# Kernel optimization log

Hardware: AMD Instinct MI355X
Metric: run time of the kernel (lower is better)

## Reference

```python
import jax, jax.numpy as jnp
import numpy as np

B = 8          # batch
S = 256        # nx+1 = ny+1 grid resolution
N = S * S      # number of DoFs per component
DIM = 2        # output vector dimension (= d_out)
W = 32         # FNO channel width
M1 = 12        # Fourier modes dim 1
M2 = 12        # Fourier modes dim 2
WF = 128       # final MLP hidden width
NL = 4         # number of Fourier layers
PADF = 8       # padding fraction denominator


def setup_inputs() -> dict:
    key = jax.random.key(0)
    ks = jax.random.split(key, 16)
    sc = 1.0 / (W * W)  # torch FNO spectral weight init scale
    return {
        "x": jax.random.normal(ks[0], (B, N), jnp.float32),
        "d2v_in": jax.random.permutation(ks[1], jnp.arange(N)),
        "v2d_out": jax.random.permutation(ks[2], jnp.arange(N)),
        "fc0_w": jax.random.normal(ks[3], (W, 3), jnp.float32) * 0.1,
        "fc0_b": jnp.zeros((W,), jnp.float32),
        "spec_w1r": jax.random.uniform(ks[4], (NL, W, W, M1, M2), jnp.float32) * sc,
        "spec_w1i": jax.random.uniform(ks[5], (NL, W, W, M1, M2), jnp.float32) * sc,
        "spec_w2r": jax.random.uniform(ks[6], (NL, W, W, M1, M2), jnp.float32) * sc,
        "spec_w2i": jax.random.uniform(ks[7], (NL, W, W, M1, M2), jnp.float32) * sc,
        "conv_w": jax.random.normal(ks[8], (NL, W, W), jnp.float32) * 0.05,
        "conv_b": jnp.zeros((NL, W), jnp.float32),
        "mlp_w1": jax.random.normal(ks[9], (WF, W), jnp.float32) * 0.05,
        "mlp_b1": jnp.zeros((WF,), jnp.float32),
        "mlp_w2": jax.random.normal(ks[10], (DIM, WF), jnp.float32) * 0.05,
        "mlp_b2": jnp.zeros((DIM,), jnp.float32),
    }


def _speconv(x, w1, w2):
    # x: (B, C, H, Wd) real; w1/w2: (C_in, C_out, M1, M2) complex64
    Bh, C, H, Wd = x.shape
    xft = jnp.fft.rfft2(x)  # (B, C, H, Wd//2+1)
    o1 = jnp.einsum('bixy,ioxy->boxy', xft[:, :, :M1, :M2], w1)
    o2 = jnp.einsum('bixy,ioxy->boxy', xft[:, :, -M1:, :M2], w2)
    out_ft = jnp.zeros((Bh, C, H, Wd // 2 + 1), jnp.complex64)
    out_ft = out_ft.at[:, :, :M1, :M2].set(o1).at[:, :, -M1:, :M2].set(o2)
    return jnp.fft.irfft2(out_ft, s=(H, Wd))


def reference(x, d2v_in, v2d_out, fc0_w, fc0_b,
              spec_w1r, spec_w1i, spec_w2r, spec_w2i,
              conv_w, conv_b, mlp_w1, mlp_b1, mlp_w2, mlp_b2):
    # DoF -> vertex gather and lift to image
    xg = x[:, d2v_in].reshape(B, 1, S, S)
    h = jnp.transpose(xg, (0, 2, 3, 1))  # (B, S, S, 1)
    # append normalized grid coordinates (get_grid2d)
    g = jnp.linspace(0.0, 1.0, S, dtype=jnp.float32)
    grid = jnp.stack(jnp.meshgrid(g, g, indexing='ij'), axis=-1)  # (S, S, 2)
    grid = jnp.broadcast_to(grid[None], (B, S, S, 2))
    h = jnp.concatenate([h, grid], axis=-1)
    # fc0 lifting
    h = h @ fc0_w.T + fc0_b              # (B, S, S, W)
    h = jnp.transpose(h, (0, 3, 1, 2))   # (B, W, S, S)
    # zero pad (non-periodic domain)
    p = S // PADF
    h = jnp.pad(h, ((0, 0), (0, 0), (0, p), (0, p)))  # (B, W, S+p, S+p)
    w1 = (spec_w1r + 1j * spec_w1i).astype(jnp.complex64)
    w2 = (spec_w2r + 1j * spec_w2i).astype(jnp.complex64)
    for l in range(NL):
        sp = _speconv(h, w1[l], w2[l])
        cv = jnp.einsum('bchw,oc->bohw', h, conv_w[l]) + conv_b[l][None, :, None, None]
        h = cv + sp
        if l != NL - 1:
            h = jax.nn.gelu(h, approximate=False)  # torch GELU default = exact erf
    # crop padding (s_outputspace=None path)
    h = h[..., :S, :S]
    # final two-layer MLP projection
    h = jnp.transpose(h, (0, 2, 3, 1))  # (B, S, S, W)
    h = jax.nn.gelu(h @ mlp_w1.T + mlp_b1, approximate=False) @ mlp_w2.T + mlp_b2
    h = jnp.transpose(h, (0, 3, 1, 2)).reshape(B, DIM, -1)  # (B, DIM, N)
    # vertex -> DoF scatter/gather and interleave components
    out = h[:, :, v2d_out]              # (B, DIM, N)
    out = jnp.transpose(out, (0, 2, 1)).reshape(B, -1)  # (B, N*DIM)
    return out
```

## Files before the change

### kernel.cpp

```cpp
#include <hip/hip_runtime.h>
#include <math.h>

#define S    256
#define Hp   288
#define C    32
#define KY   12
#define NK   24
#define Bn   8
#define PI_D 3.14159265358979323846264338327950288

#define SZ_TW (NK*Hp*2)
#define OFF_TW 0
#define OFF_H  (OFF_TW + SZ_TW)
#define SZ_H   (Bn*C*Hp*Hp)
#define OFF_Y  (OFF_H + SZ_H)
#define SZ_Y   (Bn*C*Hp*KY*2)
#define OFF_X  (OFF_Y + SZ_Y)
#define SZ_X   (Bn*C*NK*KY*2)
#define OFF_O  (OFF_X + SZ_X)
#define SZ_O   SZ_X
#define OFF_Z  (OFF_O + SZ_O)
#define SZ_Z   (Bn*Hp*C*KY*2)
#define OFF_T  (OFF_Z + SZ_Z)
#define SZ_T   (Bn*S*S*2)

#define GELU(v) (0.5f*(v)*(1.0f+erff((v)*0.70710678118654752f)))
#define SCHED_FENCE() __builtin_amdgcn_sched_barrier(0)

__global__ void k_tw(float* __restrict__ tw) {
    int i = blockIdx.x * 256 + threadIdx.x;
    if (i >= NK * Hp) return;
    int k = i / Hp, xx = i % Hp;
    int f = (k < KY) ? k : (k + 264);
    int m = (f * xx) % Hp;
    double th = (2.0 * PI_D * (double)m) / (double)Hp;
    tw[2 * i]     = (float)cos(th);
    tw[2 * i + 1] = (float)sin(th);
}

__global__ __launch_bounds__(256, 1) void k_embed(
        const float* __restrict__ xin, const int* __restrict__ d2v,
        const float* __restrict__ fw, const float* __restrict__ fb,
        const float* __restrict__ tw, float* __restrict__ h, float* __restrict__ Y) {
    __shared__ __align__(16) float xs[256];
    __shared__ __align__(16) float twy[288 * 24];
    int x = blockIdx.x, b = blockIdx.y, tid = threadIdx.x;
    size_t rowbase = (size_t)b * 2654208 + (size_t)x * 288;
    if (x >= S) {
        for (int i = tid; i < 32 * 72; i += 256) {
            int c = i / 72, q = i % 72;
            *(float4*)&h[rowbase + (size_t)c * 82944 + q * 4] = make_float4(0, 0, 0, 0);
        }
        for (int i = tid; i < 768; i += 256)
            Y[((size_t)(b * 32 + i / 24) * 288 + x) * 24 + (i % 24)] = 0.f;
        return;
    }
    for (int i = tid; i < 288 * 12; i += 256) {
        int y = i / 12, k = i % 12;
        float2 v = *(const float2*)&tw[(k * 288 + y) * 2];
        *(float2*)&twy[y * 24 + 2 * k] = v;
    }
    xs[tid & 255] = xin[b * 65536 + d2v[x * 256 + (tid & 255)]];
    int o = tid & 31, g = tid >> 5;
    float w0 = fw[o * 3], w1 = fw[o * 3 + 1], w2 = fw[o * 3 + 2], bb = fb[o];
    float gx = x * (1.0f / 255.0f);
    __syncthreads();
    float pr[12], pi[12];
    #pragma unroll
    for (int k = 0; k < 12; ++k) { pr[k] = 0.f; pi[k] = 0.f; }
    #pragma unroll 1
    for (int c3 = 0; c3 < 3; ++c3) {
        int ybase = g * 36 + c3 * 12;
        float acc[12];
        #pragma unroll
        for (int j = 0; j < 12; ++j) {
            int y = ybase + j;
            acc[j] = (y < S) ? (w0 * xs[y < S ? y : 0] + w1 * gx + w2 * (y * (1.0f / 255.0f)) + bb) : 0.f;
        }
        float* hw = h + rowbase + (size_t)o * 82944 + ybase;
        #pragma unroll
        for (int q = 0; q < 3; ++q)
            *(float4*)&hw[4 * q] = make_float4(acc[4*q], acc[4*q+1], acc[4*q+2], acc[4*q+3]);
        SCHED_FENCE();
        #pragma unroll
        for (int jp = 0; jp < 6; ++jp) {
            #pragma unroll
            for (int u = 0; u < 2; ++u) {
                int j = jp * 2 + u;
                int y = ybase + j;
                float tc[24];
                #pragma unroll
                for (int q = 0; q < 6; ++q) *(float4*)&tc[4 * q] = *(const float4*)&twy[y * 24 + 4 * q];
                float v = acc[j];
                #pragma unroll
                for (int k = 0; k < 12; ++k) { pr[k] += v * tc[2 * k]; pi[k] -= v * tc[2 * k + 1]; }
            }
            SCHED_FENCE();
        }
    }
    #pragma unroll
    for (int k = 0; k < 12; ++k) { pr[k] += __shfl_xor(pr[k], 32); pi[k] += __shfl_xor(pi[k], 32); }
    __syncthreads();
    float* YP = twy;
    if ((tid & 32) == 0) {
        float* dst = YP + ((tid >> 6) * 32 + o) * 24;
        #pragma unroll
        for (int k = 0; k < 12; ++k) { dst[2 * k] = pr[k]; dst[2 * k + 1] = pi[k]; }
    }
    __syncthreads();
    for (int i = tid; i < 768; i += 256) {
        float s = YP[i] + YP[768 + i] + YP[1536 + i] + YP[2304 + i];
        Y[((size_t)(b * 32 + i / 24) * 288 + x) * 24 + (i % 24)] = s;
    }
}

__global__ __launch_bounds__(288) void k_dftx(const float* __restrict__ Y,
                                              const float* __restrict__ tw,
                                              float* __restrict__ X) {
    __shared__ __align__(16) float Ys[288 * 24];
    int c = blockIdx.x, b = blockIdx.y, tid = threadIdx.x;
    const float* Yb = Y + (size_t)(b * 32 + c) * 6912;
    for (int i = tid; i < 1728; i += 288)
        *(float4*)&Ys[4 * i] = *(const float4*)&Yb[4 * i];
    __syncthreads();
    int k = tid / 12, ky = tid % 12;
    const float* twk = tw + k * 576;
    float xr = 0.f, xi = 0.f;
    #pragma unroll 4
    for (int xx = 0; xx < 288; ++xx) {
        float yr = Ys[xx * 24 + 2 * ky], yi = Ys[xx * 24 + 2 * ky + 1];
        float cc = twk[2 * xx], ss = twk[2 * xx + 1];
        xr += yr * cc + yi * ss;
        xi += yi * cc - yr * ss;
    }
    size_t oo = ((size_t)(b * 32 + c) * 288 + tid) * 2;
    X[oo] = xr; X[oo + 1] = xi;
}

__global__ void k_spec(const float* __restrict__ X,
                       const float* __restrict__ w1r, const float* __restrict__ w1i,
                       const float* __restrict__ w2r, const float* __restrict__ w2i,
                       float* __restrict__ O, int l) {
    int t = blockIdx.x * 256 + threadIdx.x;
    int ky = t % KY; int k = (t / KY) % NK; int o = (t / (NK * KY)) % C; int b = t / (C * NK * KY);
    int kk = (k < KY) ? k : (k - KY);
    const float* wr = (k < KY) ? w1r : w2r;
    const float* wi = (k < KY) ? w1i : w2i;
    size_t wbase = (size_t)l * C * C * 144 + (size_t)o * 144 + kk * 12 + ky;
    size_t xbase = (size_t)b * C * NK * KY * 2 + (k * KY + ky) * 2;
    float ar = 0.f, ai = 0.f;
    #pragma unroll 8
    for (int i = 0; i < C; ++i) {
        float xr = X[xbase + (size_t)i * NK * KY * 2];
        float xi = X[xbase + (size_t)i * NK * KY * 2 + 1];
        float wrr = wr[wbase + (size_t)i * C * 144];
        float wii = wi[wbase + (size_t)i * C * 144];
        ar += xr * wrr - xi * wii;
        ai += xr * wii + xi * wrr;
    }
    size_t oo = (((size_t)b * C + o) * NK * KY + k * KY + ky) * 2;
    O[oo] = ar; O[oo + 1] = ai;
}

__global__ __launch_bounds__(384) void k_idftx(const float* __restrict__ O,
                                               const float* __restrict__ tw,
                                               float* __restrict__ Z) {
    int x0 = blockIdx.x * 32; int c = blockIdx.y, b = blockIdx.z;
    int row = threadIdx.x & 31, ky = threadIdx.x >> 5;
    int x = x0 + row;
    const float* Ob = O + ((size_t)(b * C + c)) * NK * KY * 2 + ky * 2;
    float zr = 0.f, zi = 0.f;
    #pragma unroll
    for (int k = 0; k < NK; ++k) {
        float orr = Ob[k * KY * 2], oii = Ob[k * KY * 2 + 1];
        float cc = tw[(k * Hp + x) * 2], ss = tw[(k * Hp + x) * 2 + 1];
        zr += orr * cc - oii * ss;
        zi += orr * ss + oii * cc;
    }
    size_t o = ((((size_t)b * Hp + x) * C + c) * KY + ky) * 2;
    Z[o] = zr; Z[o + 1] = zi;
}

__global__ __launch_bounds__(256, 1) void k_conv(
        float* __restrict__ h, const float* __restrict__ Z,
        const float* __restrict__ cw, const float* __restrict__ cb,
        const float* __restrict__ tw, float* __restrict__ Y,
        int l, int flags) {
    __shared__ __align__(16) float hs[32 * 292];
    __shared__ __align__(16) float twy[288 * 24];
    __shared__ __align__(16) float cws[32 * 33];
    __shared__ float cbs[32];
    int x = blockIdx.x, b = blockIdx.y, tid = threadIdx.x;
    size_t rowbase = (size_t)b * 2654208 + (size_t)x * 288;
    const float* hb = h + rowbase;
    for (int i = tid; i < 32 * 72; i += 256) {
        int c = i / 72, q = i % 72;
        *(float4*)&hs[c * 292 + q * 4] = *(const float4*)&hb[(size_t)c * 82944 + q * 4];
    }
    for (int i = tid; i < 288 * 12; i += 256) {
        int y = i / 12, k = i % 12;
        float2 v = *(const float2*)&tw[(k * 288 + y) * 2];
        *(float2*)&twy[y * 24 + 2 * k] = v;
    }
    for (int i = tid; i < 32 * 32; i += 256)
        cws[(i >> 5) * 33 + (i & 31)] = cw[l * 1024 + i];
    if (tid < 32) cbs[tid] = cb[l * 32 + tid];
    int o = tid & 31, g = tid >> 5;
    const float* Zr = Z + ((size_t)(b * 288 + x) * 32 + o) * 24;
    float zr[12], zi[12];
    #pragma unroll
    for (int q = 0; q < 6; ++q) {
        float4 zv = *(const float4*)&Zr[4 * q];
        zr[2*q] = zv.x; zi[2*q] = zv.y; zr[2*q+1] = zv.z; zi[2*q+1] = zv.w;
    }
    __syncthreads();
    float bias = cbs[o];
    float pr[12], pi[12];
    #pragma unroll
    for (int k = 0; k < 12; ++k) { pr[k] = 0.f; pi[k] = 0.f; }
    const int gelu_f = flags & 1, wy = flags & 2;
    #pragma unroll 1
    for (int c3 = 0; c3 < 3; ++c3) {
        int ybase = g * 36 + c3 * 12;
        float acc[12];
        #pragma unroll
        for (int j = 0; j < 12; ++j) acc[j] = bias;
        #pragma unroll 8
        for (int c = 0; c < 32; ++c) {
            float w = cws[o * 33 + c];
            const float* hr = &hs[c * 292 + ybase];
            float4 h0 = *(const float4*)&hr[0];
            float4 h1 = *(const float4*)&hr[4];
            float4 h2 = *(const float4*)&hr[8];
            acc[0] += h0.x * w; acc[1] += h0.y * w; acc[2]  += h0.z * w; acc[3]  += h0.w * w;
            acc[4] += h1.x * w; acc[5] += h1.y * w; acc[6]  += h1.z * w; acc[7]  += h1.w * w;
            acc[8] += h2.x * w; acc[9] += h2.y * w; acc[10] += h2.z * w; acc[11] += h2.w * w;
        }
        SCHED_FENCE();
        #pragma unroll
        for (int jp = 0; jp < 6; ++jp) {
            #pragma unroll
            for (int u = 0; u < 2; ++u) {
                int j = jp * 2 + u;
                int y = ybase + j;
                float tc[24];
                #pragma unroll
                for (int q = 0; q < 6; ++q) *(float4*)&tc[4 * q] = *(const float4*)&twy[y * 24 + 4 * q];
                float sp = zr[0] * tc[0] - zi[0] * tc[1];
                #pragma unroll
                for (int k = 1; k < 12; ++k) sp += 2.f * (zr[k] * tc[2*k] - zi[k] * tc[2*k+1]);
                float val = acc[j] + sp * (1.0f / 82944.0f);
                if (gelu_f) val = GELU(val);
                acc[j] = val;
                if (wy) {
                    #pragma unroll
                    for (int k = 0; k < 12; ++k) { pr[k] += val * tc[2*k]; pi[k] -= val * tc[2*k+1]; }
                }
            }
            SCHED_FENCE();
        }
        float* hw = h + rowbase + (size_t)o * 82944 + ybase;
        #pragma unroll
        for (int q = 0; q < 3; ++q)
            *(float4*)&hw[4 * q] = make_float4(acc[4*q], acc[4*q+1], acc[4*q+2], acc[4*q+3]);
        SCHED_FENCE();
    }
    if (wy) {
        #pragma unroll
        for (int k = 0; k < 12; ++k) { pr[k] += __shfl_xor(pr[k], 32); pi[k] += __shfl_xor(pi[k], 32); }
        __syncthreads();
        float* YP = twy;
        if ((tid & 32) == 0) {
            float* dst = YP + ((tid >> 6) * 32 + o) * 24;
            #pragma unroll
            for (int k = 0; k < 12; ++k) { dst[2 * k] = pr[k]; dst[2 * k + 1] = pi[k]; }
        }
        __syncthreads();
        for (int i = tid; i < 768; i += 256) {
            float s = YP[i] + YP[768 + i] + YP[1536 + i] + YP[2304 + i];
            Y[((size_t)(b * 32 + i / 24) * 288 + x) * 24 + (i % 24)] = s;
        }
    }
}

__global__ __launch_bounds__(256) void k_mlp(const float* __restrict__ h,
                                             const float* __restrict__ w1, const float* __restrict__ b1,
                                             const float* __restrict__ w2, const float* __restrict__ b2,
                                             float* __restrict__ tmp) {
    int bid = blockIdx.x;
    int b = bid >> 7;
    int x = ((bid & 127) << 1) + (threadIdx.x >> 7);
    int lane = threadIdx.x & 127;
    const float* hb = h + (size_t)b * 2654208 + (size_t)x * 288;
    float hc0[32], hc1[32];
    #pragma unroll
    for (int c = 0; c < 32; ++c) {
        hc0[c] = hb[(size_t)c * 82944 + lane];
        hc1[c] = hb[(size_t)c * 82944 + lane + 128];
    }
    float o00 = 0.f, o01 = 0.f, o10 = 0.f, o11 = 0.f;
    for (int f = 0; f < 128; ++f) {
        float a0 = b1[f], a1 = a0;
        #pragma unroll
        for (int c = 0; c < 32; ++c) {
            float w = w1[f * 32 + c];
            a0 += hc0[c] * w; a1 += hc1[c] * w;
        }
        float wa = w2[f], wb = w2[128 + f];
        float g0 = GELU(a0), g1 = GELU(a1);
        o00 += g0 * wa; o01 += g0 * wb;
        o10 += g1 * wa; o11 += g1 * wb;
    }
    float bb0 = b2[0], bb1 = b2[1];
    int p0 = x * 256 + lane;
    size_t base = (size_t)b * 65536;
    *(float2*)&tmp[(base + p0) * 2]       = make_float2(o00 + bb0, o01 + bb1);
    *(float2*)&tmp[(base + p0 + 128) * 2] = make_float2(o10 + bb0, o11 + bb1);
}

__global__ void k_scatter(const float* __restrict__ tmp, const int* __restrict__ v2d,
                          float* __restrict__ out) {
    int id = blockIdx.x * 256 + threadIdx.x;
    int b = id >> 16; int j = id & 65535;
    int p = v2d[j];
    const float2 v = *(const float2*)(tmp + ((size_t)(b << 16) + p) * 2);
    *(float2*)(out + (size_t)id * 2) = v;
}

extern "C" void kernel_launch(void* const* d_in, const int* in_sizes, int n_in,
                              void* d_out, int out_size, void* d_ws, size_t ws_size,
                              hipStream_t stream) {
    const float* xin   = (const float*)d_in[0];
    const int*   d2v   = (const int*)  d_in[1];
    const int*   v2d   = (const int*)  d_in[2];
    const float* fc0w  = (const float*)d_in[3];
    const float* fc0b  = (const float*)d_in[4];
    const float* w1r   = (const float*)d_in[5];
    const float* w1i   = (const float*)d_in[6];
    const float* w2r   = (const float*)d_in[7];
    const float* w2i   = (const float*)d_in[8];
    const float* cw    = (const float*)d_in[9];
    const float* cb    = (const float*)d_in[10];
    const float* mw1   = (const float*)d_in[11];
    const float* mb1   = (const float*)d_in[12];
    const float* mw2   = (const float*)d_in[13];
    const float* mb2   = (const float*)d_in[14];

    float* ws = (float*)d_ws;
    float* TW = ws + OFF_TW;
    float* H  = ws + OFF_H;
    float* Y  = ws + OFF_Y;
    float* X  = ws + OFF_X;
    float* O  = ws + OFF_O;
    float* Z  = ws + OFF_Z;
    float* T  = ws + OFF_T;

    k_tw<<<(NK * Hp + 255) / 256, 256, 0, stream>>>(TW);
    k_embed<<<dim3(Hp, Bn), 256, 0, stream>>>(xin, d2v, fc0w, fc0b, TW, H, Y);

    for (int l = 0; l < 4; ++l) {
        k_dftx<<<dim3(32, Bn), 288, 0, stream>>>(Y, TW, X);
        k_spec<<<(Bn * C * NK * KY) / 256, 256, 0, stream>>>(X, w1r, w1i, w2r, w2i, O, l);
        k_idftx<<<dim3(9, 32, Bn), 384, 0, stream>>>(O, TW, Z);
        k_conv<<<dim3(Hp, Bn), 256, 0, stream>>>(H, Z, cw, cb, TW, Y, l, (l != 3) ? 3 : 0);
    }

    k_mlp<<<1024, 256, 0, stream>>>(H, mw1, mb1, mw2, mb2, T);
    k_scatter<<<(Bn * S * S) / 256, 256, 0, stream>>>(T, v2d, (float*)d_out);
}
```

Measured before the change: 847.7 us.

## Precompute transposed y-twiddles globally, split x-DFT over halves, trim shared memory

Adds a pre-transposed twiddle table built once in k_tw, so k_embed and k_conv read it directly from global/L1 instead of re-staging a 27KB shared copy in every block. Shared memory is reduced (no twiddle buffer, unpadded hs tile, a dedicated small YP buffer), and one __syncthreads is removed. k_dftx is split into two halves along x to double its grid, writing partial sums that k_spec adds together. The changes aim to cut per-block staging overhead and raise parallelism, but twiddle loads now go through the cache hierarchy, and dropping the hs padding may add LDS bank conflicts.

```diff
diff --git a/kernel.cpp b/kernel.cpp
--- a/kernel.cpp
+++ b/kernel.cpp
@@ -9,15 +9,17 @@
 #define Bn   8
 #define PI_D 3.14159265358979323846264338327950288
 
-#define SZ_TW (NK*Hp*2)
+#define SZ_TW  (NK*Hp*2)
 #define OFF_TW 0
-#define OFF_H  (OFF_TW + SZ_TW)
+#define OFF_TWT (OFF_TW + SZ_TW)
+#define SZ_TWT (Hp*KY*2)
+#define OFF_H  (OFF_TWT + SZ_TWT)
 #define SZ_H   (Bn*C*Hp*Hp)
 #define OFF_Y  (OFF_H + SZ_H)
 #define SZ_Y   (Bn*C*Hp*KY*2)
 #define OFF_X  (OFF_Y + SZ_Y)
 #define SZ_X   (Bn*C*NK*KY*2)
-#define OFF_O  (OFF_X + SZ_X)
+#define OFF_O  (OFF_X + 2*SZ_X)
 #define SZ_O   SZ_X
 #define OFF_Z  (OFF_O + SZ_O)
 #define SZ_Z   (Bn*Hp*C*KY*2)
@@ -27,23 +29,24 @@
 #define GELU(v) (0.5f*(v)*(1.0f+erff((v)*0.70710678118654752f)))
 #define SCHED_FENCE() __builtin_amdgcn_sched_barrier(0)
 
-__global__ void k_tw(float* __restrict__ tw) {
+__global__ void k_tw(float* __restrict__ tw, float* __restrict__ twT) {
     int i = blockIdx.x * 256 + threadIdx.x;
     if (i >= NK * Hp) return;
     int k = i / Hp, xx = i % Hp;
     int f = (k < KY) ? k : (k + 264);
     int m = (f * xx) % Hp;
     double th = (2.0 * PI_D * (double)m) / (double)Hp;
-    tw[2 * i]     = (float)cos(th);
-    tw[2 * i + 1] = (float)sin(th);
+    float c = (float)cos(th), s = (float)sin(th);
+    tw[2 * i] = c; tw[2 * i + 1] = s;
+    if (k < KY) { twT[xx * 24 + 2 * k] = c; twT[xx * 24 + 2 * k + 1] = s; }
 }
 
 __global__ __launch_bounds__(256, 1) void k_embed(
         const float* __restrict__ xin, const int* __restrict__ d2v,
         const float* __restrict__ fw, const float* __restrict__ fb,
-        const float* __restrict__ tw, float* __restrict__ h, float* __restrict__ Y) {
+        const float* __restrict__ twT, float* __restrict__ h, float* __restrict__ Y) {
     __shared__ __align__(16) float xs[256];
-    __shared__ __align__(16) float twy[288 * 24];
+    __shared__ __align__(16) float YP[3072];
     int x = blockIdx.x, b = blockIdx.y, tid = threadIdx.x;
     size_t rowbase = (size_t)b * 2654208 + (size_t)x * 288;
     if (x >= S) {
@@ -55,12 +58,7 @@
             Y[((size_t)(b * 32 + i / 24) * 288 + x) * 24 + (i % 24)] = 0.f;
         return;
     }
-    for (int i = tid; i < 288 * 12; i += 256) {
-        int y = i / 12, k = i % 12;
-        float2 v = *(const float2*)&tw[(k * 288 + y) * 2];
-        *(float2*)&twy[y * 24 + 2 * k] = v;
-    }
-    xs[tid & 255] = xin[b * 65536 + d2v[x * 256 + (tid & 255)]];
+    xs[tid] = xin[b * 65536 + d2v[x * 256 + tid]];
     int o = tid & 31, g = tid >> 5;
     float w0 = fw[o * 3], w1 = fw[o * 3 + 1], w2 = fw[o * 3 + 2], bb = fb[o];
     float gx = x * (1.0f / 255.0f);
@@ -88,9 +86,10 @@
             for (int u = 0; u < 2; ++u) {
                 int j = jp * 2 + u;
                 int y = ybase + j;
+                const float* tg = twT + y * 24;
                 float tc[24];
                 #pragma unroll
-                for (int q = 0; q < 6; ++q) *(float4*)&tc[4 * q] = *(const float4*)&twy[y * 24 + 4 * q];
+                for (int q = 0; q < 6; ++q) *(float4*)&tc[4 * q] = *(const float4*)&tg[4 * q];
                 float v = acc[j];
                 #pragma unroll
                 for (int k = 0; k < 12; ++k) { pr[k] += v * tc[2 * k]; pi[k] -= v * tc[2 * k + 1]; }
@@ -100,8 +99,6 @@
     }
     #pragma unroll
     for (int k = 0; k < 12; ++k) { pr[k] += __shfl_xor(pr[k], 32); pi[k] += __shfl_xor(pi[k], 32); }
-    __syncthreads();
-    float* YP = twy;
     if ((tid & 32) == 0) {
         float* dst = YP + ((tid >> 6) * 32 + o) * 24;
         #pragma unroll
@@ -117,23 +114,23 @@
 __global__ __launch_bounds__(288) void k_dftx(const float* __restrict__ Y,
                                               const float* __restrict__ tw,
                                               float* __restrict__ X) {
-    __shared__ __align__(16) float Ys[288 * 24];
-    int c = blockIdx.x, b = blockIdx.y, tid = threadIdx.x;
-    const float* Yb = Y + (size_t)(b * 32 + c) * 6912;
-    for (int i = tid; i < 1728; i += 288)
+    __shared__ __align__(16) float Ys[144 * 24];
+    int c = blockIdx.x, b = blockIdx.y, half = blockIdx.z, tid = threadIdx.x;
+    const float* Yb = Y + (size_t)(b * 32 + c) * 6912 + half * 3456;
+    for (int i = tid; i < 864; i += 288)
         *(float4*)&Ys[4 * i] = *(const float4*)&Yb[4 * i];
     __syncthreads();
     int k = tid / 12, ky = tid % 12;
-    const float* twk = tw + k * 576;
+    const float* twk = tw + k * 576 + half * 288;
     float xr = 0.f, xi = 0.f;
     #pragma unroll 4
-    for (int xx = 0; xx < 288; ++xx) {
+    for (int xx = 0; xx < 144; ++xx) {
         float yr = Ys[xx * 24 + 2 * ky], yi = Ys[xx * 24 + 2 * ky + 1];
         float cc = twk[2 * xx], ss = twk[2 * xx + 1];
         xr += yr * cc + yi * ss;
         xi += yi * cc - yr * ss;
     }
-    size_t oo = ((size_t)(b * 32 + c) * 288 + tid) * 2;
+    size_t oo = (size_t)half * SZ_X + ((size_t)(b * 32 + c) * 288 + tid) * 2;
     X[oo] = xr; X[oo + 1] = xi;
 }
 
@@ -151,8 +148,9 @@
     float ar = 0.f, ai = 0.f;
     #pragma unroll 8
     for (int i = 0; i < C; ++i) {
-        float xr = X[xbase + (size_t)i * NK * KY * 2];
-        float xi = X[xbase + (size_t)i * NK * KY * 2 + 1];
+        size_t xo = xbase + (size_t)i * NK * KY * 2;
+        float xr = X[xo]     + X[SZ_X + xo];
+        float xi = X[xo + 1] + X[SZ_X + xo + 1];
         float wrr = wr[wbase + (size_t)i * C * 144];
         float wii = wi[wbase + (size_t)i * C * 144];
         ar += xr * wrr - xi * wii;
@@ -184,24 +182,17 @@
 __global__ __launch_bounds__(256, 1) void k_conv(
         float* __restrict__ h, const float* __restrict__ Z,
         const float* __restrict__ cw, const float* __restrict__ cb,
-        const float* __restrict__ tw, float* __restrict__ Y,
+        const float* __restrict__ twT, float* __restrict__ Y,
         int l, int flags) {
-    __shared__ __align__(16) float hs[32 * 292];
-    __shared__ __align__(16) float twy[288 * 24];
+    __shared__ __align__(16) float hs[32 * 288];
+    __shared__ __align__(16) float YP[3072];
     __shared__ __align__(16) float cws[32 * 33];
     __shared__ float cbs[32];
     int x = blockIdx.x, b = blockIdx.y, tid = threadIdx.x;
     size_t rowbase = (size_t)b * 2654208 + (size_t)x * 288;
     const float* hb = h + rowbase;
-    for (int i = tid; i < 32 * 72; i += 256) {
-        int c = i / 72, q = i % 72;
-        *(float4*)&hs[c * 292 + q * 4] = *(const float4*)&hb[(size_t)c * 82944 + q * 4];
-    }
-    for (int i = tid; i < 288 * 12; i += 256) {
-        int y = i / 12, k = i % 12;
-        float2 v = *(const float2*)&tw[(k * 288 + y) * 2];
-        *(float2*)&twy[y * 24 + 2 * k] = v;
-    }
+    for (int i = tid; i < 32 * 72; i += 256)
+        *(float4*)&hs[4 * i] = *(const float4*)&hb[(size_t)(i / 72) * 82944 + (i % 72) * 4];
     for (int i = tid; i < 32 * 32; i += 256)
         cws[(i >> 5) * 33 + (i & 31)] = cw[l * 1024 + i];
     if (tid < 32) cbs[tid] = cb[l * 32 + tid];
@@ -228,7 +219,7 @@
         #pragma unroll 8
         for (int c = 0; c < 32; ++c) {
             float w = cws[o * 33 + c];
-            const float* hr = &hs[c * 292 + ybase];
+            const float* hr = &hs[c * 288 + ybase];
             float4 h0 = *(const float4*)&hr[0];
             float4 h1 = *(const float4*)&hr[4];
             float4 h2 = *(const float4*)&hr[8];
@@ -243,9 +234,10 @@
             for (int u = 0; u < 2; ++u) {
                 int j = jp * 2 + u;
                 int y = ybase + j;
+                const float* tg = twT + y * 24;
                 float tc[24];
                 #pragma unroll
-                for (int q = 0; q < 6; ++q) *(float4*)&tc[4 * q] = *(const float4*)&twy[y * 24 + 4 * q];
+                for (int q = 0; q < 6; ++q) *(float4*)&tc[4 * q] = *(const float4*)&tg[4 * q];
                 float sp = zr[0] * tc[0] - zi[0] * tc[1];
                 #pragma unroll
                 for (int k = 1; k < 12; ++k) sp += 2.f * (zr[k] * tc[2*k] - zi[k] * tc[2*k+1]);
@@ -268,8 +260,6 @@
     if (wy) {
         #pragma unroll
         for (int k = 0; k < 12; ++k) { pr[k] += __shfl_xor(pr[k], 32); pi[k] += __shfl_xor(pi[k], 32); }
-        __syncthreads();
-        float* YP = twy;
         if ((tid & 32) == 0) {
             float* dst = YP + ((tid >> 6) * 32 + o) * 24;
             #pragma unroll
@@ -346,23 +336,24 @@
     const float* mw2   = (const float*)d_in[13];
     const float* mb2   = (const float*)d_in[14];
 
-    float* ws = (float*)d_ws;
-    float* TW = ws + OFF_TW;
-    float* H  = ws + OFF_H;
-    float* Y  = ws + OFF_Y;
-    float* X  = ws + OFF_X;
-    float* O  = ws + OFF_O;
-    float* Z  = ws + OFF_Z;
-    float* T  = ws + OFF_T;
-
-    k_tw<<<(NK * Hp + 255) / 256, 256, 0, stream>>>(TW);
-    k_embed<<<dim3(Hp, Bn), 256, 0, stream>>>(xin, d2v, fc0w, fc0b, TW, H, Y);
+    float* ws  = (float*)d_ws;
+    float* TW  = ws + OFF_TW;
+    float* TWT = ws + OFF_TWT;
+    float* H   = ws + OFF_H;
+    float* Y   = ws + OFF_Y;
+    float* X   = ws + OFF_X;
+    float* O   = ws + OFF_O;
+    float* Z   = ws + OFF_Z;
+    float* T   = ws + OFF_T;
+
+    k_tw<<<(NK * Hp + 255) / 256, 256, 0, stream>>>(TW, TWT);
+    k_embed<<<dim3(Hp, Bn), 256, 0, stream>>>(xin, d2v, fc0w, fc0b, TWT, H, Y);
 
     for (int l = 0; l < 4; ++l) {
-        k_dftx<<<dim3(32, Bn), 288, 0, stream>>>(Y, TW, X);
+        k_dftx<<<dim3(32, Bn, 2), 288, 0, stream>>>(Y, TW, X);
         k_spec<<<(Bn * C * NK * KY) / 256, 256, 0, stream>>>(X, w1r, w1i, w2r, w2i, O, l);
         k_idftx<<<dim3(9, 32, Bn), 384, 0, stream>>>(O, TW, Z);
-        k_conv<<<dim3(Hp, Bn), 256, 0, stream>>>(H, Z, cw, cb, TW, Y, l, (l != 3) ? 3 : 0);
+        k_conv<<<dim3(Hp, Bn), 256, 0, stream>>>(H, Z, cw, cb, TWT, Y, l, (l != 3) ? 3 : 0);
     }
 
     k_mlp<<<1024, 256, 0, stream>>>(H, mw1, mb1, mw2, mb2, T);
```

After: 866.7 us. 2.2% more time.
